# Optimization experiments

Hardware: AMD Instinct MI355X
Metric: run time of the kernel (lower is better)

## Reference

```python
import jax, jax.numpy as jnp
import numpy as np

IN_CH = 512
RED = 8
CH = IN_CH // RED  # 64
B, H, W = 8, 64, 64


def setup_inputs() -> dict:
    key = jax.random.key(0)
    ks = jax.random.split(key, 10)
    sc_in = 1.0 / np.sqrt(IN_CH)
    sc_ch = 1.0 / np.sqrt(CH)
    return {
        "x": jax.random.normal(ks[0], (B, IN_CH, H, W), dtype=jnp.float32),
        "Wf": jax.random.uniform(ks[1], (CH, IN_CH), jnp.float32, -sc_in, sc_in),
        "bf": jax.random.uniform(ks[2], (CH,), jnp.float32, -sc_in, sc_in),
        "Wg": jax.random.uniform(ks[3], (CH, IN_CH), jnp.float32, -sc_in, sc_in),
        "bg": jax.random.uniform(ks[4], (CH,), jnp.float32, -sc_in, sc_in),
        "Wh": jax.random.uniform(ks[5], (CH, IN_CH), jnp.float32, -sc_in, sc_in),
        "bh": jax.random.uniform(ks[6], (CH,), jnp.float32, -sc_in, sc_in),
        "Wv": jax.random.uniform(ks[7], (IN_CH, CH), jnp.float32, -sc_ch, sc_ch),
        "bv": jax.random.uniform(ks[8], (IN_CH,), jnp.float32, -sc_ch, sc_ch),
        "sigma": jnp.zeros((1,), dtype=jnp.float32) + 0.5,  # nonzero so attention path is exercised
    }


def reference(x, Wf, bf, Wg, bg, Wh, bh, Wv, bv, sigma):
    b, c, h, w = x.shape
    xt = x.reshape(b, c, h * w).transpose(0, 2, 1)  # [b, N, c]
    ff = xt @ Wf.T + bf                              # [b, N, ch]
    fg = xt @ Wg.T + bg                              # [b, N, ch]
    s = jax.nn.softmax(jnp.einsum("bnd,bmd->bnm", ff, fg), axis=-1)  # [b, N, N]
    fh = xt @ Wh.T + bh                              # [b, N, ch]
    fv = jnp.einsum("bnm,bmd->bnd", s, fh) @ Wv.T + bv  # [b, N, c]
    return x + sigma * fv.transpose(0, 2, 1).reshape(b, c, h, w)
```

## Files before the change

kernel.cpp:

```cpp
#include <hip/hip_runtime.h>
#include <hip/hip_bf16.h>
#include <stdint.h>

#define BATCH 8
#define NN 4096
#define DD 64
#define CC 512
#define SPLIT 4
#define NT (NN / SPLIT / 64)
#define LOG2E 1.44269504088896f

using f32x4   = __attribute__((ext_vector_type(4))) float;
using f32x16  = __attribute__((ext_vector_type(16))) float;
using bf16x8  = __attribute__((ext_vector_type(8))) short;

__device__ __forceinline__ uint16_t f2bf(float f) {
  union { float f; uint32_t u; } v; v.f = f;
  uint32_t r = v.u + 0x7fffu + ((v.u >> 16) & 1u);
  return (uint16_t)(r >> 16);
}
__device__ __forceinline__ float bf2f(uint16_t h) {
  union { uint32_t u; float f; } v; v.u = ((uint32_t)h) << 16;
  return v.f;
}
__device__ __forceinline__ uint32_t cvtpk(float a, float b) {
  uint32_t r;
  asm("v_cvt_pk_bf16_f32 %0, %1, %2" : "=v"(r) : "v"(a), "v"(b));
  return r;
}
__device__ __forceinline__ float exp2a(float x) {
  float r;
  asm("v_exp_f32 %0, %1" : "=v"(r) : "v"(x));
  return r;
}

__device__ __forceinline__ void gload16(const void* g, void* l) {
  __builtin_amdgcn_global_load_lds((const __attribute__((address_space(1))) void*)g,
                                   (__attribute__((address_space(3))) void*)l, 16, 0, 0);
}

__global__ void cvt_w_kernel(const float* __restrict__ Wf, const float* __restrict__ Wg,
                             const float* __restrict__ Wh, const float* __restrict__ Wv,
                             uint16_t* __restrict__ Wb, uint16_t* __restrict__ Wvb) {
  int i = blockIdx.x * 256 + threadIdx.x;
  if (i < 3 * 64 * 512) {
    int p = i >> 15, r = i & 32767, ch = r >> 9, c = r & 511;
    const float* W = (p == 0) ? Wf : (p == 1) ? Wg : Wh;
    int slot = ((c >> 3) & 7) ^ (ch & 7);
    Wb[(size_t)(p * 64 + ch) * 512 + (c >> 6) * 64 + slot * 8 + (c & 7)] = f2bf(W[ch * 512 + c]);
  } else if (i < 3 * 64 * 512 + 512 * 64) {
    int j = i - 3 * 64 * 512;
    Wvb[j] = f2bf(Wv[j]);
  }
}

__global__ __launch_bounds__(256) void proj_kernel(
    const float* __restrict__ x, const uint16_t* __restrict__ Wb,
    const float* __restrict__ bfp, const float* __restrict__ bgp, const float* __restrict__ bhp,
    uint16_t* __restrict__ Qb, uint16_t* __restrict__ Kb, uint16_t* __restrict__ Vt) {
  const int bid = blockIdx.x;
  const int b = bid >> 6, nt = bid & 63, n0 = nt * 64;
  const int t = threadIdx.x, w = t >> 6, lane = t & 63;
  const int l5 = lane >> 5, lm = lane & 31;

  __shared__ uint16_t xl[2][64 * 64];
  __shared__ uint16_t wl[2][192 * 64];

  const float* xp = x + (size_t)b * CC * NN + n0;
  const int nB0 = (w & 1) * 32, ch0w = (w >> 1) * 32;

  f32x16 acc[3];
#pragma unroll
  for (int p = 0; p < 3; ++p)
#pragma unroll
    for (int q = 0; q < 16; ++q) acc[p][q] = 0.f;

  float xr[16];

  auto stageW = [&](int buf, int k) {
#pragma unroll
    for (int i = 0; i < 6; ++i) {
      int e = t + i * 256;
      const uint16_t* src = Wb + (size_t)(e >> 3) * 512 + k * 64 + (e & 7) * 8;
      gload16(src, &wl[buf][(size_t)(w * 64 + i * 256) * 8]);
    }
  };
  auto loadX = [&](int k) {
#pragma unroll
    for (int r = 0; r < 2; ++r)
#pragma unroll
      for (int j = 0; j < 8; ++j)
        xr[r * 8 + j] = xp[(size_t)(k * 64 + r * 32 + w * 8 + j) * NN + lane];
  };
  auto writeX = [&](int buf) {
#pragma unroll
    for (int r = 0; r < 2; ++r) {
      int slot = (r * 4 + w) ^ (lane & 7);
      uint4 v;
      v.x = cvtpk(xr[r * 8 + 0], xr[r * 8 + 1]);
      v.y = cvtpk(xr[r * 8 + 2], xr[r * 8 + 3]);
      v.z = cvtpk(xr[r * 8 + 4], xr[r * 8 + 5]);
      v.w = cvtpk(xr[r * 8 + 6], xr[r * 8 + 7]);
      *(uint4*)&xl[buf][lane * 64 + slot * 8] = v;
    }
  };

  stageW(0, 0);
  loadX(0);
  writeX(0);
  __syncthreads();

  for (int k = 0; k < 8; ++k) {
    const int buf = k & 1;
    if (k < 7) { loadX(k + 1); stageW(buf ^ 1, k + 1); }
#pragma unroll
    for (int ks = 0; ks < 4; ++ks) {
      const int slot = (ks * 2 + l5) ^ (lm & 7);
      bf16x8 bfrag = *(const bf16x8*)&xl[buf][(nB0 + lm) * 64 + slot * 8];
#pragma unroll
      for (int p = 0; p < 3; ++p) {
        bf16x8 afrag = *(const bf16x8*)&wl[buf][(size_t)(p * 64 + ch0w + lm) * 64 + slot * 8];
        acc[p] = __builtin_amdgcn_mfma_f32_32x32x16_bf16(afrag, bfrag, acc[p], 0, 0, 0);
      }
    }
    if (k < 7) writeX(buf ^ 1);
    __syncthreads();
  }

  const int nG = n0 + nB0 + lm;
  const float* biasP[3] = {bfp, bgp, bhp};
#pragma unroll
  for (int p = 0; p < 2; ++p) {
    uint16_t* dst = (p == 0 ? Qb : Kb) + ((size_t)b * NN + nG) * DD;
    const float scl = (p == 0) ? LOG2E : 1.0f;
#pragma unroll
    for (int g = 0; g < 4; ++g) {
      const int chb = ch0w + 4 * l5 + 8 * g;
      uint2 v;
      v.x = cvtpk((acc[p][g * 4 + 0] + biasP[p][chb + 0]) * scl,
                  (acc[p][g * 4 + 1] + biasP[p][chb + 1]) * scl);
      v.y = cvtpk((acc[p][g * 4 + 2] + biasP[p][chb + 2]) * scl,
                  (acc[p][g * 4 + 3] + biasP[p][chb + 3]) * scl);
      *(uint2*)&dst[chb] = v;
    }
  }
  {
    uint16_t* dst = Vt + (size_t)b * DD * NN + nG;
#pragma unroll
    for (int q = 0; q < 16; ++q) {
      const int d = ch0w + 4 * l5 + 8 * (q >> 2) + (q & 3);
      dst[(size_t)d * NN] = f2bf(acc[2][q] + bhp[d]);
    }
  }
}

__global__ __launch_bounds__(256, 4) void flash_kernel(
    const uint16_t* __restrict__ Qb, const uint16_t* __restrict__ Kb,
    const uint16_t* __restrict__ Vt,
    float* __restrict__ lpart, uint16_t* __restrict__ opart) {
  const int bid = blockIdx.x;
  const int wid = (bid & 7) * 128 + (bid >> 3);
  const int qt = wid & 31;
  const int z  = (wid >> 5) & 3;
  const int b  = wid >> 7;
  const int tid  = threadIdx.x;
  const int wave = tid >> 6, lane = tid & 63;
  const int l31 = lane & 31, h = lane >> 5, rx = lane & 7;

  __shared__ uint16_t kv_lds[2][2][64 * 64];

  const int q0w = qt * 128 + wave * 32;
  bf16x8 qf[4];
  {
    const uint16_t* Qp = Qb + ((size_t)b * NN + q0w + l31) * DD + h * 8;
#pragma unroll
    for (int ks = 0; ks < 4; ++ks) qf[ks] = *(const bf16x8*)(Qp + ks * 16);
  }

  const uint16_t* Kbase = Kb + (size_t)b * NN * DD;
  const uint16_t* Vbase = Vt + (size_t)b * DD * NN;
  const int kvstart = z * (NN / SPLIT);

  const int srow = wave * 16 + (lane >> 3);
  const int csw  = (lane & 7) ^ ((lane >> 3) & 7);
  auto stage = [&](int buf, int kv0) {
    uint16_t* kl = &kv_lds[buf][0][0] + wave * 1024;
    uint16_t* vl = &kv_lds[buf][1][0] + wave * 1024;
    gload16(Kbase + ((size_t)kv0 + srow) * DD + csw * 8,     kl);
    gload16(Kbase + ((size_t)kv0 + srow + 8) * DD + csw * 8, kl + 512);
    gload16(Vbase + (size_t)srow * NN + kv0 + csw * 8,       vl);
    gload16(Vbase + (size_t)(srow + 8) * NN + kv0 + csw * 8, vl + 512);
  };

  f32x16 o0 = {}, o1 = {};
  f32x4 lacc = {0.f, 0.f, 0.f, 0.f};

  stage(0, kvstart);
  __syncthreads();

  int cur = 0;
  for (int it = 0; it < NT; ++it) {
    if (it + 1 < NT) stage(cur ^ 1, kvstart + (it + 1) * 64);
    const uint16_t* klds = &kv_lds[cur][0][0];
    const uint16_t* vlds = &kv_lds[cur][1][0];

    f32x16 s0, s1;
    {
      const uint16_t* kr0 = klds + l31 * 64;
      const uint16_t* kr1 = klds + (32 + l31) * 64;
      f32x16 a0 = {}, a1 = {};
      __builtin_amdgcn_s_setprio(1);
#pragma unroll
      for (int ks = 0; ks < 4; ++ks) {
        bf16x8 ka = *(const bf16x8*)(kr0 + (((ks * 2 + h) ^ rx) * 8));
        a0 = __builtin_amdgcn_mfma_f32_32x32x16_bf16(ka, qf[ks], a0, 0, 0, 0);
      }
#pragma unroll
      for (int ks = 0; ks < 4; ++ks) {
        bf16x8 ka = *(const bf16x8*)(kr1 + (((ks * 2 + h) ^ rx) * 8));
        a1 = __builtin_amdgcn_mfma_f32_32x32x16_bf16(ka, qf[ks], a1, 0, 0, 0);
      }
      __builtin_amdgcn_s_setprio(0);
      s0 = a0; s1 = a1;
    }

#pragma unroll
    for (int q = 0; q < 16; ++q) s0[q] = exp2a(s0[q]);
#pragma unroll
    for (int q = 0; q < 16; ++q) s1[q] = exp2a(s1[q]);
#pragma unroll
    for (int q = 0; q < 16; ++q) lacc[q & 3] += s0[q];
#pragma unroll
    for (int q = 0; q < 16; ++q) lacc[q & 3] += s1[q];

    uint32_t pbu[4][4];
#pragma unroll
    for (int r2 = 0; r2 < 4; ++r2) {
      pbu[0][r2] = cvtpk(s0[2 * r2],     s0[2 * r2 + 1]);
      pbu[1][r2] = cvtpk(s0[8 + 2 * r2], s0[9 + 2 * r2]);
      pbu[2][r2] = cvtpk(s1[2 * r2],     s1[2 * r2 + 1]);
      pbu[3][r2] = cvtpk(s1[8 + 2 * r2], s1[9 + 2 * r2]);
    }
#pragma unroll
    for (int f = 0; f < 4; ++f) {
      asm volatile("v_permlane32_swap_b32 %0, %1" : "+v"(pbu[f][0]), "+v"(pbu[f][2]));
      asm volatile("v_permlane32_swap_b32 %0, %1" : "+v"(pbu[f][1]), "+v"(pbu[f][3]));
    }

    union UF { uint32_t u[4]; bf16x8 v; };
    {
      const uint16_t* vr = vlds + l31 * 64;
      __builtin_amdgcn_s_setprio(1);
#pragma unroll
      for (int kk = 0; kk < 4; ++kk) {
        bf16x8 va = *(const bf16x8*)(vr + (((kk * 2 + h) ^ rx) * 8));
        UF pf; pf.u[0] = pbu[kk][0]; pf.u[1] = pbu[kk][1];
               pf.u[2] = pbu[kk][2]; pf.u[3] = pbu[kk][3];
        o0 = __builtin_amdgcn_mfma_f32_32x32x16_bf16(va, pf.v, o0, 0, 0, 0);
      }
      __builtin_amdgcn_s_setprio(0);
    }
    {
      const uint16_t* vr = vlds + (32 + l31) * 64;
      __builtin_amdgcn_s_setprio(1);
#pragma unroll
      for (int kk = 0; kk < 4; ++kk) {
        bf16x8 va = *(const bf16x8*)(vr + (((kk * 2 + h) ^ rx) * 8));
        UF pf; pf.u[0] = pbu[kk][0]; pf.u[1] = pbu[kk][1];
               pf.u[2] = pbu[kk][2]; pf.u[3] = pbu[kk][3];
        o1 = __builtin_amdgcn_mfma_f32_32x32x16_bf16(va, pf.v, o1, 0, 0, 0);
      }
      __builtin_amdgcn_s_setprio(0);
    }

    __syncthreads();
    cur ^= 1;
  }

  float rs = lacc[0] + lacc[1] + lacc[2] + lacc[3];
  rs += __shfl_xor(rs, 32, 64);
  const float invl = 1.0f / rs;
  if (h == 0) lpart[((size_t)b * NN + q0w + l31) * SPLIT + z] = rs;

  uint16_t* op = opart + (((size_t)b * NN + q0w + l31) * SPLIT + z) * DD;
#pragma unroll
  for (int r2 = 0; r2 < 8; ++r2) {
    uint32_t w0 = cvtpk(o0[2 * r2] * invl, o0[2 * r2 + 1] * invl);
    uint32_t w1 = cvtpk(o1[2 * r2] * invl, o1[2 * r2 + 1] * invl);
    const int d0 = (r2 >> 1) * 8 + (r2 & 1) * 2 + 4 * h;
    *(uint32_t*)&op[d0]      = w0;
    *(uint32_t*)&op[32 + d0] = w1;
  }
}

__global__ __launch_bounds__(256) void combine_kernel(
    const float* __restrict__ lpart, const uint16_t* __restrict__ opart,
    const uint16_t* __restrict__ Wvb, const float* __restrict__ bv,
    const float* __restrict__ x, const float* __restrict__ sigma,
    float* __restrict__ out) {
  const int qt = blockIdx.x;
  const int b  = blockIdx.y;
  const int t    = threadIdx.x;
  const int wave = t >> 6;
  const int lane = t & 63;
  const int lg   = lane >> 4;
  const int lm   = lane & 15;

  __shared__ uint16_t plds[4][16][72];
  uint16_t (*plw)[72] = plds[wave];

  const int qrow = qt * 64 + wave * 16 + lm;
  const size_t base4 = ((size_t)b * NN + qrow) * SPLIT;

  float lv[SPLIT], tot = 0.f;
#pragma unroll
  for (int i = 0; i < SPLIT; ++i) { lv[i] = lpart[base4 + i]; tot += lv[i]; }
  const float inv = 1.0f / tot;
  float wgt[SPLIT];
#pragma unroll
  for (int i = 0; i < SPLIT; ++i) wgt[i] = lv[i] * inv;

  const uint16_t* obase = opart + base4 * DD;
#pragma unroll
  for (int k = 0; k < 4; ++k) {
    const int d0 = lg * 16 + k * 4;
    float a0 = 0.f, a1 = 0.f, a2 = 0.f, a3 = 0.f;
#pragma unroll
    for (int i = 0; i < SPLIT; ++i) {
      uint2 r = *(const uint2*)&obase[(size_t)i * DD + d0];
      a0 += bf2f(r.x & 0xffff) * wgt[i];
      a1 += bf2f(r.x >> 16)    * wgt[i];
      a2 += bf2f(r.y & 0xffff) * wgt[i];
      a3 += bf2f(r.y >> 16)    * wgt[i];
    }
    uint2 wv2;
    wv2.x = cvtpk(a0, a1);
    wv2.y = cvtpk(a2, a3);
    *(uint2*)&plw[lm][d0] = wv2;
  }
  asm volatile("s_waitcnt lgkmcnt(0)" ::: "memory");
  __builtin_amdgcn_sched_barrier(0);
  bf16x8 oa0 = *(const bf16x8*)&plw[lm][8 * lg];
  bf16x8 oa1 = *(const bf16x8*)&plw[lm][32 + 8 * lg];

  const float sg = sigma[0];
  const float* xb = x   + (size_t)b * CC * NN;
  float*       ob = out + (size_t)b * CC * NN;
  const int qr = qt * 64 + wave * 16 + lg * 4;

#pragma unroll 4
  for (int tc2 = 0; tc2 < 32; ++tc2) {
    const int c = tc2 * 16 + lm;
    const uint16_t* Wp = Wvb + (size_t)c * DD + lg * 8;
    bf16x8 wb0 = *(const bf16x8*)Wp;
    bf16x8 wb1 = *(const bf16x8*)(Wp + 32);
    f32x4 a = {0.f, 0.f, 0.f, 0.f};
    a = __builtin_amdgcn_mfma_f32_16x16x32_bf16(oa0, wb0, a, 0, 0, 0);
    a = __builtin_amdgcn_mfma_f32_16x16x32_bf16(oa1, wb1, a, 0, 0, 0);
    const float bvc = bv[c];
    size_t base = (size_t)c * NN + qr;
    f32x4 xv = *(const f32x4*)(xb + base);
    f32x4 ov;
#pragma unroll
    for (int r = 0; r < 4; ++r) ov[r] = xv[r] + sg * (a[r] + bvc);
    *(f32x4*)(ob + base) = ov;
  }
}

extern "C" void kernel_launch(void* const* d_in, const int* in_sizes, int n_in,
                              void* d_out, int out_size, void* d_ws, size_t ws_size,
                              hipStream_t stream) {
  const float* x   = (const float*)d_in[0];
  const float* Wf  = (const float*)d_in[1];
  const float* bfp = (const float*)d_in[2];
  const float* Wg  = (const float*)d_in[3];
  const float* bgp = (const float*)d_in[4];
  const float* Wh  = (const float*)d_in[5];
  const float* bhp = (const float*)d_in[6];
  const float* Wv  = (const float*)d_in[7];
  const float* bv  = (const float*)d_in[8];
  const float* sg  = (const float*)d_in[9];
  float* out = (float*)d_out;

  const size_t nqk = (size_t)BATCH * NN * DD;
  uint16_t* Qb   = (uint16_t*)d_ws;
  uint16_t* Kb   = Qb + nqk;
  uint16_t* Vt   = Kb + nqk;
  uint16_t* Wvb  = Vt + nqk;
  uint16_t* Wb   = Wvb + (size_t)CC * DD;
  float* lpart   = (float*)(Wb + (size_t)3 * 64 * 512);
  uint16_t* opart = (uint16_t*)(lpart + (size_t)BATCH * NN * SPLIT);

  hipLaunchKernelGGL(cvt_w_kernel, dim3(512), dim3(256), 0, stream, Wf, Wg, Wh, Wv, Wb, Wvb);
  hipLaunchKernelGGL(proj_kernel, dim3(512), dim3(256), 0, stream,
                     x, Wb, bfp, bgp, bhp, Qb, Kb, Vt);
  hipLaunchKernelGGL(flash_kernel, dim3(1024), dim3(256), 0, stream,
                     Qb, Kb, Vt, lpart, opart);
  hipLaunchKernelGGL(combine_kernel, dim3(NN / 64, BATCH), dim3(256), 0, stream,
                     lpart, opart, Wvb, bv, x, sg, out);
}
```

Before: 103.1 us.

## Process 64 query rows per wave in flash kernel to reuse K/V fragments

Each wave now handles two 32-row query sub-tiles instead of one, so every K and V fragment loaded from LDS feeds two MFMAs. The block tile grows to 256 queries and the grid is halved to 512 blocks. The goal is to cut LDS read traffic and global K/V staging per query. The cost is roughly double the accumulator and Q registers, and the occupancy hint in launch_bounds is dropped. That lowers occupancy, and 512 blocks may underfill the device.

```diff
diff --git a/kernel.cpp b/kernel.cpp
--- a/kernel.cpp
+++ b/kernel.cpp
@@ -154,27 +154,28 @@
   }
 }
 
-__global__ __launch_bounds__(256, 4) void flash_kernel(
+__global__ __launch_bounds__(256) void flash_kernel(
     const uint16_t* __restrict__ Qb, const uint16_t* __restrict__ Kb,
     const uint16_t* __restrict__ Vt,
     float* __restrict__ lpart, uint16_t* __restrict__ opart) {
   const int bid = blockIdx.x;
-  const int wid = (bid & 7) * 128 + (bid >> 3);
-  const int qt = wid & 31;
-  const int z  = (wid >> 5) & 3;
-  const int b  = wid >> 7;
+  const int wid = (bid & 7) * 64 + (bid >> 3);
+  const int qt = wid & 15;
+  const int z  = (wid >> 4) & 3;
+  const int b  = wid >> 6;
   const int tid  = threadIdx.x;
   const int wave = tid >> 6, lane = tid & 63;
   const int l31 = lane & 31, h = lane >> 5, rx = lane & 7;
 
   __shared__ uint16_t kv_lds[2][2][64 * 64];
 
-  const int q0w = qt * 128 + wave * 32;
-  bf16x8 qf[4];
-  {
-    const uint16_t* Qp = Qb + ((size_t)b * NN + q0w + l31) * DD + h * 8;
-#pragma unroll
-    for (int ks = 0; ks < 4; ++ks) qf[ks] = *(const bf16x8*)(Qp + ks * 16);
+  const int q0w = qt * 256 + wave * 64;
+  bf16x8 qf[2][4];
+#pragma unroll
+  for (int u = 0; u < 2; ++u) {
+    const uint16_t* Qp = Qb + ((size_t)b * NN + q0w + u * 32 + l31) * DD + h * 8;
+#pragma unroll
+    for (int ks = 0; ks < 4; ++ks) qf[u][ks] = *(const bf16x8*)(Qp + ks * 16);
   }
 
   const uint16_t* Kbase = Kb + (size_t)b * NN * DD;
@@ -192,8 +193,8 @@
     gload16(Vbase + (size_t)(srow + 8) * NN + kv0 + csw * 8, vl + 512);
   };
 
-  f32x16 o0 = {}, o1 = {};
-  f32x4 lacc = {0.f, 0.f, 0.f, 0.f};
+  f32x16 o00 = {}, o01 = {}, o10 = {}, o11 = {};
+  f32x4 lac0 = {0.f, 0.f, 0.f, 0.f}, lac1 = {0.f, 0.f, 0.f, 0.f};
 
   stage(0, kvstart);
   __syncthreads();
@@ -204,92 +205,94 @@
     const uint16_t* klds = &kv_lds[cur][0][0];
     const uint16_t* vlds = &kv_lds[cur][1][0];
 
-    f32x16 s0, s1;
-    {
-      const uint16_t* kr0 = klds + l31 * 64;
-      const uint16_t* kr1 = klds + (32 + l31) * 64;
-      f32x16 a0 = {}, a1 = {};
+    bf16x8 ka[2][4];
+#pragma unroll
+    for (int t2 = 0; t2 < 2; ++t2) {
+      const uint16_t* kr = klds + (t2 * 32 + l31) * 64;
+#pragma unroll
+      for (int ks = 0; ks < 4; ++ks)
+        ka[t2][ks] = *(const bf16x8*)(kr + (((ks * 2 + h) ^ rx) * 8));
+    }
+
+    uint32_t pbu[2][4][4];
+#pragma unroll
+    for (int u = 0; u < 2; ++u) {
+      f32x16 s0 = {}, s1 = {};
       __builtin_amdgcn_s_setprio(1);
 #pragma unroll
-      for (int ks = 0; ks < 4; ++ks) {
-        bf16x8 ka = *(const bf16x8*)(kr0 + (((ks * 2 + h) ^ rx) * 8));
-        a0 = __builtin_amdgcn_mfma_f32_32x32x16_bf16(ka, qf[ks], a0, 0, 0, 0);
+      for (int ks = 0; ks < 4; ++ks)
+        s0 = __builtin_amdgcn_mfma_f32_32x32x16_bf16(ka[0][ks], qf[u][ks], s0, 0, 0, 0);
+#pragma unroll
+      for (int ks = 0; ks < 4; ++ks)
+        s1 = __builtin_amdgcn_mfma_f32_32x32x16_bf16(ka[1][ks], qf[u][ks], s1, 0, 0, 0);
+      __builtin_amdgcn_s_setprio(0);
+#pragma unroll
+      for (int q = 0; q < 16; ++q) s0[q] = exp2a(s0[q]);
+#pragma unroll
+      for (int q = 0; q < 16; ++q) s1[q] = exp2a(s1[q]);
+      f32x4& lac = u ? lac1 : lac0;
+#pragma unroll
+      for (int q = 0; q < 16; ++q) lac[q & 3] += s0[q] + s1[q];
+#pragma unroll
+      for (int r2 = 0; r2 < 4; ++r2) {
+        pbu[u][0][r2] = cvtpk(s0[2 * r2],     s0[2 * r2 + 1]);
+        pbu[u][1][r2] = cvtpk(s0[8 + 2 * r2], s0[9 + 2 * r2]);
+        pbu[u][2][r2] = cvtpk(s1[2 * r2],     s1[2 * r2 + 1]);
+        pbu[u][3][r2] = cvtpk(s1[8 + 2 * r2], s1[9 + 2 * r2]);
       }
 #pragma unroll
-      for (int ks = 0; ks < 4; ++ks) {
-        bf16x8 ka = *(const bf16x8*)(kr1 + (((ks * 2 + h) ^ rx) * 8));
-        a1 = __builtin_amdgcn_mfma_f32_32x32x16_bf16(ka, qf[ks], a1, 0, 0, 0);
+      for (int f = 0; f < 4; ++f) {
+        asm volatile("v_permlane32_swap_b32 %0, %1" : "+v"(pbu[u][f][0]), "+v"(pbu[u][f][2]));
+        asm volatile("v_permlane32_swap_b32 %0, %1" : "+v"(pbu[u][f][1]), "+v"(pbu[u][f][3]));
+      }
+    }
+
+    union UF { uint32_t u4[4]; bf16x8 v; };
+#pragma unroll
+    for (int dt = 0; dt < 2; ++dt) {
+      const uint16_t* vr = vlds + (dt * 32 + l31) * 64;
+      __builtin_amdgcn_s_setprio(1);
+#pragma unroll
+      for (int kk = 0; kk < 4; ++kk) {
+        bf16x8 va = *(const bf16x8*)(vr + (((kk * 2 + h) ^ rx) * 8));
+        UF p0; p0.u4[0] = pbu[0][kk][0]; p0.u4[1] = pbu[0][kk][1];
+               p0.u4[2] = pbu[0][kk][2]; p0.u4[3] = pbu[0][kk][3];
+        UF p1; p1.u4[0] = pbu[1][kk][0]; p1.u4[1] = pbu[1][kk][1];
+               p1.u4[2] = pbu[1][kk][2]; p1.u4[3] = pbu[1][kk][3];
+        if (dt == 0) {
+          o00 = __builtin_amdgcn_mfma_f32_32x32x16_bf16(va, p0.v, o00, 0, 0, 0);
+          o10 = __builtin_amdgcn_mfma_f32_32x32x16_bf16(va, p1.v, o10, 0, 0, 0);
+        } else {
+          o01 = __builtin_amdgcn_mfma_f32_32x32x16_bf16(va, p0.v, o01, 0, 0, 0);
+          o11 = __builtin_amdgcn_mfma_f32_32x32x16_bf16(va, p1.v, o11, 0, 0, 0);
+        }
       }
       __builtin_amdgcn_s_setprio(0);
-      s0 = a0; s1 = a1;
-    }
-
-#pragma unroll
-    for (int q = 0; q < 16; ++q) s0[q] = exp2a(s0[q]);
-#pragma unroll
-    for (int q = 0; q < 16; ++q) s1[q] = exp2a(s1[q]);
-#pragma unroll
-    for (int q = 0; q < 16; ++q) lacc[q & 3] += s0[q];
-#pragma unroll
-    for (int q = 0; q < 16; ++q) lacc[q & 3] += s1[q];
-
-    uint32_t pbu[4][4];
-#pragma unroll
-    for (int r2 = 0; r2 < 4; ++r2) {
-      pbu[0][r2] = cvtpk(s0[2 * r2],     s0[2 * r2 + 1]);
-      pbu[1][r2] = cvtpk(s0[8 + 2 * r2], s0[9 + 2 * r2]);
-      pbu[2][r2] = cvtpk(s1[2 * r2],     s1[2 * r2 + 1]);
-      pbu[3][r2] = cvtpk(s1[8 + 2 * r2], s1[9 + 2 * r2]);
-    }
-#pragma unroll
-    for (int f = 0; f < 4; ++f) {
-      asm volatile("v_permlane32_swap_b32 %0, %1" : "+v"(pbu[f][0]), "+v"(pbu[f][2]));
-      asm volatile("v_permlane32_swap_b32 %0, %1" : "+v"(pbu[f][1]), "+v"(pbu[f][3]));
-    }
-
-    union UF { uint32_t u[4]; bf16x8 v; };
-    {
-      const uint16_t* vr = vlds + l31 * 64;
-      __builtin_amdgcn_s_setprio(1);
-#pragma unroll
-      for (int kk = 0; kk < 4; ++kk) {
-        bf16x8 va = *(const bf16x8*)(vr + (((kk * 2 + h) ^ rx) * 8));
-        UF pf; pf.u[0] = pbu[kk][0]; pf.u[1] = pbu[kk][1];
-               pf.u[2] = pbu[kk][2]; pf.u[3] = pbu[kk][3];
-        o0 = __builtin_amdgcn_mfma_f32_32x32x16_bf16(va, pf.v, o0, 0, 0, 0);
-      }
-      __builtin_amdgcn_s_setprio(0);
-    }
-    {
-      const uint16_t* vr = vlds + (32 + l31) * 64;
-      __builtin_amdgcn_s_setprio(1);
-#pragma unroll
-      for (int kk = 0; kk < 4; ++kk) {
-        bf16x8 va = *(const bf16x8*)(vr + (((kk * 2 + h) ^ rx) * 8));
-        UF pf; pf.u[0] = pbu[kk][0]; pf.u[1] = pbu[kk][1];
-               pf.u[2] = pbu[kk][2]; pf.u[3] = pbu[kk][3];
-        o1 = __builtin_amdgcn_mfma_f32_32x32x16_bf16(va, pf.v, o1, 0, 0, 0);
-      }
-      __builtin_amdgcn_s_setprio(0);
     }
 
     __syncthreads();
     cur ^= 1;
   }
 
-  float rs = lacc[0] + lacc[1] + lacc[2] + lacc[3];
-  rs += __shfl_xor(rs, 32, 64);
-  const float invl = 1.0f / rs;
-  if (h == 0) lpart[((size_t)b * NN + q0w + l31) * SPLIT + z] = rs;
-
-  uint16_t* op = opart + (((size_t)b * NN + q0w + l31) * SPLIT + z) * DD;
-#pragma unroll
-  for (int r2 = 0; r2 < 8; ++r2) {
-    uint32_t w0 = cvtpk(o0[2 * r2] * invl, o0[2 * r2 + 1] * invl);
-    uint32_t w1 = cvtpk(o1[2 * r2] * invl, o1[2 * r2 + 1] * invl);
-    const int d0 = (r2 >> 1) * 8 + (r2 & 1) * 2 + 4 * h;
-    *(uint32_t*)&op[d0]      = w0;
-    *(uint32_t*)&op[32 + d0] = w1;
+#pragma unroll
+  for (int u = 0; u < 2; ++u) {
+    f32x4& lac = u ? lac1 : lac0;
+    float rs = lac[0] + lac[1] + lac[2] + lac[3];
+    rs += __shfl_xor(rs, 32, 64);
+    const float invl = 1.0f / rs;
+    const int qg = q0w + u * 32 + l31;
+    if (h == 0) lpart[((size_t)b * NN + qg) * SPLIT + z] = rs;
+    uint16_t* op = opart + (((size_t)b * NN + qg) * SPLIT + z) * DD;
+    f32x16& a0 = u ? o10 : o00;
+    f32x16& a1 = u ? o11 : o01;
+#pragma unroll
+    for (int r2 = 0; r2 < 8; ++r2) {
+      uint32_t w0 = cvtpk(a0[2 * r2] * invl, a0[2 * r2 + 1] * invl);
+      uint32_t w1 = cvtpk(a1[2 * r2] * invl, a1[2 * r2 + 1] * invl);
+      const int d0 = (r2 >> 1) * 8 + (r2 & 1) * 2 + 4 * h;
+      *(uint32_t*)&op[d0]      = w0;
+      *(uint32_t*)&op[32 + d0] = w1;
+    }
   }
 }
 
@@ -394,7 +397,7 @@
   hipLaunchKernelGGL(cvt_w_kernel, dim3(512), dim3(256), 0, stream, Wf, Wg, Wh, Wv, Wb, Wvb);
   hipLaunchKernelGGL(proj_kernel, dim3(512), dim3(256), 0, stream,
                      x, Wb, bfp, bgp, bhp, Qb, Kb, Vt);
-  hipLaunchKernelGGL(flash_kernel, dim3(1024), dim3(256), 0, stream,
+  hipLaunchKernelGGL(flash_kernel, dim3(512), dim3(256), 0, stream,
                      Qb, Kb, Vt, lpart, opart);
   hipLaunchKernelGGL(combine_kernel, dim3(NN / 64, BATCH), dim3(256), 0, stream,
                      lpart, opart, Wvb, bv, x, sg, out);
```

After: 103.8 us. Within noise of the previous version (+0.7%).

## Load V fragments directly from global memory instead of staging through LDS

Applied to the files above, without the earlier changes.

V tiles are no longer staged into shared memory. Each wave reads its V fragments straight from global memory into registers each iteration, which halves LDS usage and drops the V staging loads. K fragments are now preloaded from LDS in one batch before the QK MFMAs, and the PV MFMAs for the two output tiles are interleaved. The launch-bounds occupancy hint is also removed. In exchange, every wave re-reads V from global or L2 with no reuse across waves and with exposed load latency inside the loop, and register pressure goes up.

```diff
diff --git a/kernel.cpp b/kernel.cpp
--- a/kernel.cpp
+++ b/kernel.cpp
@@ -154,7 +154,7 @@
   }
 }
 
-__global__ __launch_bounds__(256, 4) void flash_kernel(
+__global__ __launch_bounds__(256) void flash_kernel(
     const uint16_t* __restrict__ Qb, const uint16_t* __restrict__ Kb,
     const uint16_t* __restrict__ Vt,
     float* __restrict__ lpart, uint16_t* __restrict__ opart) {
@@ -167,7 +167,7 @@
   const int wave = tid >> 6, lane = tid & 63;
   const int l31 = lane & 31, h = lane >> 5, rx = lane & 7;
 
-  __shared__ uint16_t kv_lds[2][2][64 * 64];
+  __shared__ uint16_t k_lds[2][64 * 64];
 
   const int q0w = qt * 128 + wave * 32;
   bf16x8 qf[4];
@@ -184,13 +184,13 @@
   const int srow = wave * 16 + (lane >> 3);
   const int csw  = (lane & 7) ^ ((lane >> 3) & 7);
   auto stage = [&](int buf, int kv0) {
-    uint16_t* kl = &kv_lds[buf][0][0] + wave * 1024;
-    uint16_t* vl = &kv_lds[buf][1][0] + wave * 1024;
+    uint16_t* kl = &k_lds[buf][0] + wave * 1024;
     gload16(Kbase + ((size_t)kv0 + srow) * DD + csw * 8,     kl);
     gload16(Kbase + ((size_t)kv0 + srow + 8) * DD + csw * 8, kl + 512);
-    gload16(Vbase + (size_t)srow * NN + kv0 + csw * 8,       vl);
-    gload16(Vbase + (size_t)(srow + 8) * NN + kv0 + csw * 8, vl + 512);
   };
+
+  const uint16_t* vg0 = Vbase + (size_t)(l31) * NN + kvstart;
+  const uint16_t* vg1 = Vbase + (size_t)(32 + l31) * NN + kvstart;
 
   f32x16 o0 = {}, o1 = {};
   f32x4 lacc = {0.f, 0.f, 0.f, 0.f};
@@ -201,27 +201,32 @@
   int cur = 0;
   for (int it = 0; it < NT; ++it) {
     if (it + 1 < NT) stage(cur ^ 1, kvstart + (it + 1) * 64);
-    const uint16_t* klds = &kv_lds[cur][0][0];
-    const uint16_t* vlds = &kv_lds[cur][1][0];
-
-    f32x16 s0, s1;
-    {
-      const uint16_t* kr0 = klds + l31 * 64;
-      const uint16_t* kr1 = klds + (32 + l31) * 64;
-      f32x16 a0 = {}, a1 = {};
-      __builtin_amdgcn_s_setprio(1);
-#pragma unroll
-      for (int ks = 0; ks < 4; ++ks) {
-        bf16x8 ka = *(const bf16x8*)(kr0 + (((ks * 2 + h) ^ rx) * 8));
-        a0 = __builtin_amdgcn_mfma_f32_32x32x16_bf16(ka, qf[ks], a0, 0, 0, 0);
-      }
-#pragma unroll
-      for (int ks = 0; ks < 4; ++ks) {
-        bf16x8 ka = *(const bf16x8*)(kr1 + (((ks * 2 + h) ^ rx) * 8));
-        a1 = __builtin_amdgcn_mfma_f32_32x32x16_bf16(ka, qf[ks], a1, 0, 0, 0);
-      }
-      __builtin_amdgcn_s_setprio(0);
-      s0 = a0; s1 = a1;
+    const uint16_t* klds = &k_lds[cur][0];
+
+    bf16x8 ka[2][4];
+#pragma unroll
+    for (int t2 = 0; t2 < 2; ++t2) {
+      const uint16_t* kr = klds + (t2 * 32 + l31) * 64;
+#pragma unroll
+      for (int ks = 0; ks < 4; ++ks)
+        ka[t2][ks] = *(const bf16x8*)(kr + (((ks * 2 + h) ^ rx) * 8));
+    }
+
+    f32x16 s0 = {}, s1 = {};
+    __builtin_amdgcn_s_setprio(1);
+#pragma unroll
+    for (int ks = 0; ks < 4; ++ks)
+      s0 = __builtin_amdgcn_mfma_f32_32x32x16_bf16(ka[0][ks], qf[ks], s0, 0, 0, 0);
+#pragma unroll
+    for (int ks = 0; ks < 4; ++ks)
+      s1 = __builtin_amdgcn_mfma_f32_32x32x16_bf16(ka[1][ks], qf[ks], s1, 0, 0, 0);
+    __builtin_amdgcn_s_setprio(0);
+
+    bf16x8 va[2][4];
+#pragma unroll
+    for (int kk = 0; kk < 4; ++kk) {
+      va[0][kk] = *(const bf16x8*)(vg0 + (kk * 2 + h) * 8);
+      va[1][kk] = *(const bf16x8*)(vg1 + (kk * 2 + h) * 8);
     }
 
 #pragma unroll
@@ -229,9 +234,7 @@
 #pragma unroll
     for (int q = 0; q < 16; ++q) s1[q] = exp2a(s1[q]);
 #pragma unroll
-    for (int q = 0; q < 16; ++q) lacc[q & 3] += s0[q];
-#pragma unroll
-    for (int q = 0; q < 16; ++q) lacc[q & 3] += s1[q];
+    for (int q = 0; q < 16; ++q) lacc[q & 3] += s0[q] + s1[q];
 
     uint32_t pbu[4][4];
 #pragma unroll
@@ -247,32 +250,18 @@
       asm volatile("v_permlane32_swap_b32 %0, %1" : "+v"(pbu[f][1]), "+v"(pbu[f][3]));
     }
 
-    union UF { uint32_t u[4]; bf16x8 v; };
-    {
-      const uint16_t* vr = vlds + l31 * 64;
-      __builtin_amdgcn_s_setprio(1);
-#pragma unroll
-      for (int kk = 0; kk < 4; ++kk) {
-        bf16x8 va = *(const bf16x8*)(vr + (((kk * 2 + h) ^ rx) * 8));
-        UF pf; pf.u[0] = pbu[kk][0]; pf.u[1] = pbu[kk][1];
-               pf.u[2] = pbu[kk][2]; pf.u[3] = pbu[kk][3];
-        o0 = __builtin_amdgcn_mfma_f32_32x32x16_bf16(va, pf.v, o0, 0, 0, 0);
-      }
-      __builtin_amdgcn_s_setprio(0);
-    }
-    {
-      const uint16_t* vr = vlds + (32 + l31) * 64;
-      __builtin_amdgcn_s_setprio(1);
-#pragma unroll
-      for (int kk = 0; kk < 4; ++kk) {
-        bf16x8 va = *(const bf16x8*)(vr + (((kk * 2 + h) ^ rx) * 8));
-        UF pf; pf.u[0] = pbu[kk][0]; pf.u[1] = pbu[kk][1];
-               pf.u[2] = pbu[kk][2]; pf.u[3] = pbu[kk][3];
-        o1 = __builtin_amdgcn_mfma_f32_32x32x16_bf16(va, pf.v, o1, 0, 0, 0);
-      }
-      __builtin_amdgcn_s_setprio(0);
-    }
-
+    union UF { uint32_t u4[4]; bf16x8 v; };
+    __builtin_amdgcn_s_setprio(1);
+#pragma unroll
+    for (int kk = 0; kk < 4; ++kk) {
+      UF pf; pf.u4[0] = pbu[kk][0]; pf.u4[1] = pbu[kk][1];
+             pf.u4[2] = pbu[kk][2]; pf.u4[3] = pbu[kk][3];
+      o0 = __builtin_amdgcn_mfma_f32_32x32x16_bf16(va[0][kk], pf.v, o0, 0, 0, 0);
+      o1 = __builtin_amdgcn_mfma_f32_32x32x16_bf16(va[1][kk], pf.v, o1, 0, 0, 0);
+    }
+    __builtin_amdgcn_s_setprio(0);
+
+    vg0 += 64; vg1 += 64;
     __syncthreads();
     cur ^= 1;
   }
```

Result: slower. 129.7 us (+25.7%).
